# Kernel tuning notes

Measured on AMD Instinct MI355X. Metric: run time of the kernel, lower is better.

The kernel has to match this reference:

```python
import jax, jax.numpy as jnp
import numpy as np

D_MODEL = 1024
NUM_HEADS = 16
DIM_Q = 1024
DIM_K = DIM_Q // NUM_HEADS  # 64, also dim_v
B, S = 2, 2048


def setup_inputs() -> dict:
    key = jax.random.key(0)
    ks = jax.random.split(key, 11)
    sd = 0.02
    return {
        "inputs_q": jax.random.normal(ks[0], (B, S, D_MODEL), dtype=jnp.float32),
        "inputs_k": jax.random.normal(ks[1], (B, S, D_MODEL), dtype=jnp.float32),
        "inputs_v": jax.random.normal(ks[2], (B, S, D_MODEL), dtype=jnp.float32),
        "Wq": jax.random.normal(ks[3], (D_MODEL, DIM_Q), dtype=jnp.float32) * sd,
        "bq": jax.random.normal(ks[4], (DIM_Q,), dtype=jnp.float32) * sd,
        "Wk": jax.random.normal(ks[5], (D_MODEL, DIM_K), dtype=jnp.float32) * sd,
        "bk": jax.random.normal(ks[6], (DIM_K,), dtype=jnp.float32) * sd,
        "Wv": jax.random.normal(ks[7], (D_MODEL, DIM_K), dtype=jnp.float32) * sd,
        "bv": jax.random.normal(ks[8], (DIM_K,), dtype=jnp.float32) * sd,
        "Wo": jax.random.normal(ks[9], (DIM_K * NUM_HEADS, D_MODEL), dtype=jnp.float32) * sd,
        "bo": jax.random.normal(ks[10], (D_MODEL,), dtype=jnp.float32) * sd,
    }


def reference(inputs_q, inputs_k, inputs_v, Wq, bq, Wk, bk, Wv, bv, Wo, bo):
    q = inputs_q @ Wq + bq                       # [B, S, dim_q]
    k = inputs_k @ Wk + bk                       # [B, S, dim_k] (single shared head)
    v = inputs_v @ Wv + bv                       # [B, S, dim_v]
    b, n, _ = q.shape
    q = q.reshape(b, n, NUM_HEADS, DIM_K).transpose(0, 2, 1, 3)  # [B, H, N, dk]
    logits = jnp.einsum("bhnk,bmk->bhnm", q, k) / jnp.sqrt(jnp.float32(DIM_K))
    # causal mask (lower triangular keep)
    causal = jnp.tril(jnp.ones((n, k.shape[1]), dtype=bool))
    logits = jnp.where(causal[None, None], logits, -jnp.inf)
    attn = jax.nn.softmax(logits, axis=-1)
    out = jnp.einsum("bhnm,bmv->bhnv", attn, v)  # [B, H, N, dv]
    out = out.transpose(0, 2, 1, 3).reshape(b, n, NUM_HEADS * DIM_K)
    return out @ Wo + bo
```

## Files before the change

kernel.cpp:

```cpp
#include <hip/hip_runtime.h>
#include <cstdint>
#include <cstddef>

typedef unsigned short u16;
typedef __bf16 bf16x8 __attribute__((ext_vector_type(8)));
typedef float  f32x4  __attribute__((ext_vector_type(4)));
typedef float  f32x16 __attribute__((ext_vector_type(16)));
typedef unsigned u32x4 __attribute__((ext_vector_type(4)));

#define DEV __device__ __forceinline__

#define B_  2
#define S_  2048
#define DM  1024
#define H_  16
#define DK  64
#define M_  (B_ * S_)

#if __has_builtin(__builtin_amdgcn_exp2f)
#define EXP2(x) __builtin_amdgcn_exp2f(x)
#else
#define EXP2(x) exp2f(x)
#endif

constexpr size_t OFF_QBF  = 0;
constexpr size_t OFF_KF   = OFF_QBF  + (size_t)M_ * DM * 2;
constexpr size_t OFF_VF   = OFF_KF   + (size_t)M_ * DK * 2;
constexpr size_t OFF_AOBF = OFF_VF   + (size_t)M_ * DK * 2;
constexpr size_t OFF_WQT  = OFF_AOBF + (size_t)M_ * DM * 2;
constexpr size_t OFF_WOT  = OFF_WQT  + (size_t)DM * DM * 2;
constexpr size_t OFF_WKT  = OFF_WOT  + (size_t)DM * DM * 2;
constexpr size_t OFF_WVT  = OFF_WKT  + (size_t)DK * DM * 2;
constexpr size_t OFF_XQBF = OFF_WVT  + (size_t)DK * DM * 2;

DEV u16 f2bf(float f) {
  unsigned u = __float_as_uint(f);
  u += 0x7fffu + ((u >> 16) & 1u);
  return (u16)(u >> 16);
}

DEV unsigned cvtpk(float lo, float hi) {
  return (unsigned)f2bf(lo) | ((unsigned)f2bf(hi) << 16);
}

DEV unsigned cvtpk_hw(float lo, float hi) {
  unsigned r;
  asm("v_cvt_pk_bf16_f32 %0, %1, %2" : "=v"(r) : "v"(lo), "v"(hi));
  return r;
}

DEV u32x4 pack8(const float4& a, const float4& b) {
  u32x4 w;
  w[0] = cvtpk(a.x, a.y);
  w[1] = cvtpk(a.z, a.w);
  w[2] = cvtpk(b.x, b.y);
  w[3] = cvtpk(b.z, b.w);
  return w;
}

DEV void gload_lds16(const void* g, void* l) {
  __builtin_amdgcn_global_load_lds(
      (const __attribute__((address_space(1))) unsigned int*)g,
      (__attribute__((address_space(3))) unsigned int*)l, 16, 0, 0);
}

struct GemmSmem { u16 At[2][128 * 64]; u16 Bt[2][64 * 64]; };
struct KvSmem   { u16 At[64 * 32]; u16 Bt[64 * 32]; u16 stage[64][72]; };
union QkvSmem { GemmSmem g; KvSmem kv; };

__global__ __launch_bounds__(256) void prep_kernel(
    const float* __restrict__ Wq, const float* __restrict__ Wo,
    const float* __restrict__ Wk, const float* __restrict__ Wv,
    const float* __restrict__ in_q,
    u16* __restrict__ WqT, u16* __restrict__ WoT,
    u16* __restrict__ WkT, u16* __restrict__ WvT,
    u16* __restrict__ Xq) {
  const int z = blockIdx.z;
  if (z == 4) {
    const int tid = (blockIdx.y * 32 + blockIdx.x) * 256 +
                    threadIdx.y * 32 + threadIdx.x;
    const int n8 = M_ * DM / 8;
    for (int i = tid; i < n8; i += 1024 * 256) {
      float4 a = ((const float4*)in_q)[2 * i];
      float4 b = ((const float4*)in_q)[2 * i + 1];
      ((u32x4*)Xq)[i] = pack8(a, b);
    }
    return;
  }
  const float* W; u16* WT; int C;
  if (z == 0)      { W = Wq; WT = WqT; C = DM; }
  else if (z == 1) { W = Wo; WT = WoT; C = DM; }
  else if (z == 2) { W = Wk; WT = WkT; C = DK; }
  else             { W = Wv; WT = WvT; C = DK; }
  const int c0 = blockIdx.x * 32, r0 = blockIdx.y * 32;
  if (c0 >= C) return;
  __shared__ u16 tile[32][33];
  for (int i = threadIdx.y; i < 32; i += 8)
    tile[i][threadIdx.x] = f2bf(W[(size_t)(r0 + i) * C + c0 + threadIdx.x]);
  __syncthreads();
  for (int i = threadIdx.y; i < 32; i += 8)
    WT[(size_t)(c0 + i) * DM + r0 + threadIdx.x] = tile[threadIdx.x][i];
}

DEV void kvproj_dev(KvSmem& sm,
                    const float* __restrict__ X, const u16* __restrict__ WT,
                    const float* __restrict__ bias,
                    u16* __restrict__ KF, u16* __restrict__ VF,
                    int bm, int sel) {
  const int tid = threadIdx.x, wave = tid >> 6, lane = tid & 63;
  const int g = lane >> 4, c = lane & 15;
  const int wm = wave >> 1, wn = wave & 1;
  f32x4 acc[2][2] = {};

  const int row = tid >> 2, sd = tid & 3;
  const float* Asrc = X + (size_t)(bm * 64 + row) * DM + sd * 8;
  const u16* Bsrc = WT + (size_t)row * DM + ((sd ^ (row & 3)) * 8);
  u16* Adst = sm.At + row * 32 + ((sd ^ (row & 3)) * 8);

  for (int k0 = 0; k0 < DM; k0 += 32) {
    __syncthreads();
    const float4 x0 = *(const float4*)(Asrc + k0);
    const float4 x1 = *(const float4*)(Asrc + k0 + 4);
    gload_lds16(Bsrc + k0, sm.Bt + wave * 512);
    *(u32x4*)Adst = pack8(x0, x1);
    asm volatile("s_waitcnt vmcnt(0)" ::: "memory");
    __syncthreads();

    bf16x8 af[2], bfr[2];
#pragma unroll
    for (int mf = 0; mf < 2; ++mf) {
      const int ra = wm * 32 + mf * 16 + c;
      af[mf] = *(const bf16x8*)(sm.At + ra * 32 + ((g ^ (ra & 3)) * 8));
    }
#pragma unroll
    for (int nf = 0; nf < 2; ++nf) {
      const int rb = wn * 32 + nf * 16 + c;
      bfr[nf] = *(const bf16x8*)(sm.Bt + rb * 32 + ((g ^ (rb & 3)) * 8));
    }
#pragma unroll
    for (int mf = 0; mf < 2; ++mf)
#pragma unroll
      for (int nf = 0; nf < 2; ++nf)
        acc[mf][nf] = __builtin_amdgcn_mfma_f32_16x16x32_bf16(
            af[mf], bfr[nf], acc[mf][nf], 0, 0, 0);
  }

  __syncthreads();
#pragma unroll
  for (int nf = 0; nf < 2; ++nf) {
    const int col = wn * 32 + nf * 16 + c;
    const float bs = bias[col];
#pragma unroll
    for (int mf = 0; mf < 2; ++mf)
#pragma unroll
      for (int r = 0; r < 4; ++r)
        sm.stage[wm * 32 + mf * 16 + g * 4 + r][col] = f2bf(acc[mf][nf][r] + bs);
  }
  __syncthreads();

  u16* outF = (sel ? VF : KF) + (size_t)bm * 4096;
#pragma unroll
  for (int p = 0; p < 2; ++p) {
    const int id = tid + p * 256;
    const int sub = id >> 8, ks = (id >> 6) & 3, ln = id & 63;
    const int hi2 = ln >> 5, q = ln & 31;
    if (!sel) {
      const int sq = (q & ~12) | ((q & 4) << 1) | ((q & 8) >> 1);
      *(bf16x8*)&outF[id * 8] =
          *(const bf16x8*)&sm.stage[sub * 32 + sq][ks * 16 + hi2 * 8];
    } else {
      u16 tmp[8];
#pragma unroll
      for (int i = 0; i < 8; ++i)
        tmp[i] = sm.stage[ks * 16 + hi2 * 8 + i][sub * 32 + q];
      *(bf16x8*)&outF[id * 8] = *(const bf16x8*)tmp;
    }
  }
}

template <int OUT_F32>
DEV void gemm_dev(GemmSmem& sm,
                  const u16* __restrict__ A, const u16* __restrict__ BT,
                  const float* __restrict__ bias, void* __restrict__ Cout,
                  int M, int N, int K, float oscale, int bm, int bn) {
  const int tid = threadIdx.x, wave = tid >> 6, lane = tid & 63;
  const int wm = wave >> 1, wn = wave & 1;
  const int g = lane >> 4, c = lane & 15;
  f32x4 acc[4][2] = {};

  int arow[4], acol[4], brow[2], bcol[2];
#pragma unroll
  for (int i = 0; i < 4; ++i) {
    const int sid = (i * 4 + wave) * 64 + lane;
    arow[i] = sid >> 3;
    acol[i] = ((sid & 7) ^ ((sid >> 3) & 7)) * 8;
  }
#pragma unroll
  for (int i = 0; i < 2; ++i) {
    const int sid = (i * 4 + wave) * 64 + lane;
    brow[i] = sid >> 3;
    bcol[i] = ((sid & 7) ^ ((sid >> 3) & 7)) * 8;
  }
  const int nt = K >> 6;

  auto stage_g = [&](int buf, int t) {
    const int k0_ = t << 6;
#pragma unroll
    for (int i = 0; i < 4; ++i)
      gload_lds16(A + (size_t)(bm * 128 + arow[i]) * K + k0_ + acol[i],
                  &sm.At[buf][(i * 4 + wave) * 512]);
#pragma unroll
    for (int i = 0; i < 2; ++i)
      gload_lds16(BT + (size_t)(bn * 64 + brow[i]) * K + k0_ + bcol[i],
                  &sm.Bt[buf][(i * 4 + wave) * 512]);
  };

  stage_g(0, 0);
  asm volatile("s_waitcnt vmcnt(0)" ::: "memory");
  __syncthreads();

  int cur = 0;
  for (int t = 0; t < nt; ++t) {
    if (t + 1 < nt) stage_g(cur ^ 1, t + 1);
#pragma unroll
    for (int kk = 0; kk < 2; ++kk) {
      bf16x8 af[4], bfr[2];
#pragma unroll
      for (int mf = 0; mf < 4; ++mf) {
        const int row = wm * 64 + mf * 16 + c;
        af[mf] = *(const bf16x8*)(&sm.At[cur][row * 64 + ((kk * 4 + g) ^ (row & 7)) * 8]);
      }
#pragma unroll
      for (int nf = 0; nf < 2; ++nf) {
        const int row = wn * 32 + nf * 16 + c;
        bfr[nf] = *(const bf16x8*)(&sm.Bt[cur][row * 64 + ((kk * 4 + g) ^ (row & 7)) * 8]);
      }
#pragma unroll
      for (int mf = 0; mf < 4; ++mf)
#pragma unroll
        for (int nf = 0; nf < 2; ++nf)
          acc[mf][nf] = __builtin_amdgcn_mfma_f32_16x16x32_bf16(
              af[mf], bfr[nf], acc[mf][nf], 0, 0, 0);
    }
    asm volatile("s_waitcnt vmcnt(0)" ::: "memory");
    __syncthreads();
    cur ^= 1;
  }

  const int colb = bn * 64 + wn * 32 + c;
  const int rowb = bm * 128 + wm * 64 + g * 4;
#pragma unroll
  for (int nf = 0; nf < 2; ++nf) {
    float bs = bias[colb + nf * 16];
#pragma unroll
    for (int mf = 0; mf < 4; ++mf) {
#pragma unroll
      for (int r = 0; r < 4; ++r) {
        size_t idx = (size_t)(rowb + mf * 16 + r) * N + colb + nf * 16;
        float v = (acc[mf][nf][r] + bs) * oscale;
        if (OUT_F32) ((float*)Cout)[idx] = v;
        else         ((u16*)Cout)[idx]   = f2bf(v);
      }
    }
  }
}

__global__ __launch_bounds__(256) void qkv_fused_kernel(
    const u16* __restrict__ Xq, const u16* __restrict__ WqT,
    const float* __restrict__ bq, u16* __restrict__ Qbf, float qscale,
    const float* __restrict__ Xk, const float* __restrict__ Xv,
    const u16* __restrict__ WkT, const u16* __restrict__ WvT,
    const float* __restrict__ bk, const float* __restrict__ bv,
    u16* __restrict__ KF, u16* __restrict__ VF) {
  __shared__ QkvSmem sm;
  if (blockIdx.y < 16) {
    gemm_dev<0>(sm.g, Xq, WqT, bq, Qbf, M_, DM, DM, qscale,
                blockIdx.x, blockIdx.y);
  } else {
    const int id = (blockIdx.y - 16) * 32 + blockIdx.x;
    const int sel = id >> 6, bm = id & 63;
    kvproj_dev(sm.kv, sel ? Xv : Xk, sel ? WvT : WkT, sel ? bv : bk,
               KF, VF, bm, sel);
  }
}

template <int OUT_F32>
__global__ __launch_bounds__(256) void gemm_bf16_kernel(
    const u16* __restrict__ A, const u16* __restrict__ BT,
    const float* __restrict__ bias, void* __restrict__ Cout,
    int M, int N, int K, float oscale) {
  __shared__ GemmSmem sm;
  gemm_dev<OUT_F32>(sm, A, BT, bias, Cout, M, N, K, oscale,
                    blockIdx.x, blockIdx.y);
}

DEV void attn_load(const u16* kp, const u16* vp, bf16x8* kf, bf16x8* vf) {
#pragma unroll
  for (int i = 0; i < 4; ++i) {
    kf[i]     = *(const bf16x8*)(kp + i * 512);
    kf[4 + i] = *(const bf16x8*)(kp + 2048 + i * 512);
    vf[i]     = *(const bf16x8*)(vp + i * 512);
    vf[4 + i] = *(const bf16x8*)(vp + 2048 + i * 512);
  }
}

DEV void attn_comp(int t, int qrow, int hi, bool evenU, int nt,
                   const bf16x8* kf, const bf16x8* vf, const bf16x8* qf,
                   f32x16& acc0, f32x16& acc1, float& l_) {
  const int kv0 = t * 64;
  const bool diag = (t == nt - 1);
  const bool skipHi = diag && evenU;

  f32x16 sf0 = {}, sf1 = {};
  __builtin_amdgcn_s_setprio(1);
#pragma unroll
  for (int ks = 0; ks < 4; ++ks)
    sf0 = __builtin_amdgcn_mfma_f32_32x32x16_bf16(kf[ks], qf[ks], sf0, 0, 0, 0);
  if (!skipHi) {
#pragma unroll
    for (int ks = 0; ks < 4; ++ks)
      sf1 = __builtin_amdgcn_mfma_f32_32x32x16_bf16(kf[4 + ks], qf[ks], sf1, 0, 0, 0);
  }
  __builtin_amdgcn_s_setprio(0);

  if (diag) {
#pragma unroll
    for (int r = 0; r < 16; ++r) {
      const int kvl = (r & 7) + 8 * hi + 16 * (r >> 3);
      if (kv0 + kvl > qrow)      sf0[r] = -1e30f;
      if (kv0 + 32 + kvl > qrow) sf1[r] = -1e30f;
    }
  }

  float rs0 = 0.f, rs1 = 0.f;
#pragma unroll
  for (int r = 0; r < 8; ++r)  { float e = EXP2(sf0[r]); sf0[r] = e; rs0 += e; }
#pragma unroll
  for (int r = 8; r < 16; ++r) { float e = EXP2(sf0[r]); sf0[r] = e; rs1 += e; }
  if (!skipHi) {
#pragma unroll
    for (int r = 0; r < 8; ++r)  { float e = EXP2(sf1[r]); sf1[r] = e; rs0 += e; }
#pragma unroll
    for (int r = 8; r < 16; ++r) { float e = EXP2(sf1[r]); sf1[r] = e; rs1 += e; }
  }
  l_ += rs0 + rs1;

  __builtin_amdgcn_s_setprio(1);
#pragma unroll
  for (int at = 0; at < 2; ++at) {
    if (at == 1 && skipHi) break;
    const f32x16& sfv = at ? sf1 : sf0;
#pragma unroll
    for (int half = 0; half < 2; ++half) {
      const int rb = half * 8;
      u32x4 pw;
      pw[0] = cvtpk_hw(sfv[rb + 0], sfv[rb + 1]);
      pw[1] = cvtpk_hw(sfv[rb + 2], sfv[rb + 3]);
      pw[2] = cvtpk_hw(sfv[rb + 4], sfv[rb + 5]);
      pw[3] = cvtpk_hw(sfv[rb + 6], sfv[rb + 7]);
      const bf16x8 pa = __builtin_bit_cast(bf16x8, pw);
      const int ksg = at * 2 + half;
      acc0 = __builtin_amdgcn_mfma_f32_32x32x16_bf16(pa, vf[ksg], acc0, 0, 0, 0);
      acc1 = __builtin_amdgcn_mfma_f32_32x32x16_bf16(pa, vf[4 + ksg], acc1, 0, 0, 0);
    }
  }
  __builtin_amdgcn_s_setprio(0);
}

__global__ __launch_bounds__(128, 2) void attn_kernel(
    const u16* __restrict__ Q,
    const u16* __restrict__ KF,
    const u16* __restrict__ VF,
    u16* __restrict__ O) {
  __shared__ float Ll[2][32];
  __shared__ float Lacc[2][32][64];

  const int j = blockIdx.x, h = blockIdx.y, b = blockIdx.z;
  const int wave = threadIdx.x >> 6, lane = threadIdx.x & 63;
  const int q31 = lane & 31, hi = lane >> 5;

  const int u = 63 - j;
  const int qrow = u * 32 + q31;
  const int nt = (u + 2) >> 1;
  const bool evenU = !(u & 1);

  const u16* Qp = Q + (size_t)(b * S_ + qrow) * DM + h * DK;
  bf16x8 qf[4];
#pragma unroll
  for (int ks = 0; ks < 4; ++ks)
    qf[ks] = *(const bf16x8*)(Qp + ks * 16 + hi * 8);

  f32x16 acc0 = {}, acc1 = {};
  float l_ = 0.f;

  const u16* kfb = KF + (size_t)(b * 32) * 4096 + lane * 8;
  const u16* vfb = VF + (size_t)(b * 32) * 4096 + lane * 8;

  bf16x8 kA[8], vA[8], kB[8], vB[8];
  int t = wave;
  if (t < nt)
    attn_load(kfb + (size_t)t * 4096, vfb + (size_t)t * 4096, kA, vA);
  for (; t < nt; t += 4) {
    const int t1 = t + 2;
    if (t1 < nt)
      attn_load(kfb + (size_t)t1 * 4096, vfb + (size_t)t1 * 4096, kB, vB);
    attn_comp(t, qrow, hi, evenU, nt, kA, vA, qf, acc0, acc1, l_);
    if (t1 < nt) {
      const int t2 = t1 + 2;
      if (t2 < nt)
        attn_load(kfb + (size_t)t2 * 4096, vfb + (size_t)t2 * 4096, kA, vA);
      attn_comp(t1, qrow, hi, evenU, nt, kB, vB, qf, acc0, acc1, l_);
    }
  }

  l_ += __shfl_xor(l_, 32);

  if (hi == 0) Ll[wave][q31] = l_;
  __syncthreads();

#pragma unroll
  for (int r = 0; r < 16; ++r) {
    const int rr = (r & 3) + 8 * (r >> 2) + 4 * hi;
    Lacc[wave][rr][q31]      = acc0[r];
    Lacc[wave][rr][32 + q31] = acc1[r];
  }
  __syncthreads();

  const int tid = threadIdx.x;
  const int row = tid >> 2;
  const int dv0 = (tid & 3) * 16;
  const float Lr = Ll[0][row] + Ll[1][row];
  const float linv = 1.f / Lr;
  u16 ov[16];
#pragma unroll
  for (int i = 0; i < 16; ++i) {
    const float v = (Lacc[0][row][dv0 + i] + Lacc[1][row][dv0 + i]) * linv;
    ov[i] = f2bf(v);
  }
  u16* Op = O + (size_t)(b * S_ + u * 32 + row) * DM + h * DK + dv0;
  *(bf16x8*)Op       = *(const bf16x8*)ov;
  *(bf16x8*)(Op + 8) = *(const bf16x8*)(ov + 8);
}

extern "C" void kernel_launch(void* const* d_in, const int* in_sizes, int n_in,
                              void* d_out, int out_size, void* d_ws, size_t ws_size,
                              hipStream_t stream) {
  const float* in_q = (const float*)d_in[0];
  const float* in_k = (const float*)d_in[1];
  const float* in_v = (const float*)d_in[2];
  const float* Wq   = (const float*)d_in[3];
  const float* bq   = (const float*)d_in[4];
  const float* Wk   = (const float*)d_in[5];
  const float* bk   = (const float*)d_in[6];
  const float* Wv   = (const float*)d_in[7];
  const float* bv   = (const float*)d_in[8];
  const float* Wo   = (const float*)d_in[9];
  const float* bo   = (const float*)d_in[10];

  char* ws  = (char*)d_ws;
  u16* Qbf  = (u16*)(ws + OFF_QBF);
  u16* KFp  = (u16*)(ws + OFF_KF);
  u16* VFp  = (u16*)(ws + OFF_VF);
  u16* AObf = (u16*)(ws + OFF_AOBF);
  u16* WqT  = (u16*)(ws + OFF_WQT);
  u16* WoT  = (u16*)(ws + OFF_WOT);
  u16* WkT  = (u16*)(ws + OFF_WKT);
  u16* WvT  = (u16*)(ws + OFF_WVT);
  u16* Xqbf = (u16*)(ws + OFF_XQBF);

  prep_kernel<<<dim3(32, 32, 5), dim3(32, 8), 0, stream>>>(
      Wq, Wo, Wk, Wv, in_q, WqT, WoT, WkT, WvT, Xqbf);

  qkv_fused_kernel<<<dim3(32, 20), 256, 0, stream>>>(
      Xqbf, WqT, bq, Qbf, 0.125f * 1.44269504088896f,
      in_k, in_v, WkT, WvT, bk, bv, KFp, VFp);

  attn_kernel<<<dim3(64, H_, B_), 128, 0, stream>>>(Qbf, KFp, VFp, AObf);

  gemm_bf16_kernel<1><<<dim3(M_ / 128, DM / 64), 256, 0, stream>>>(
      AObf, WoT, bo, d_out, M_, DM, DM, 1.0f);
}
```

Measured before the change: 95.09 us.

## Double-buffer K/V projection GEMM with 64-wide K tiles and prefetch

Result: no change. 93.81 us (-1.4%).

```diff
diff --git a/kernel.cpp b/kernel.cpp
--- a/kernel.cpp
+++ b/kernel.cpp
@@ -65,7 +65,7 @@
 }
 
 struct GemmSmem { u16 At[2][128 * 64]; u16 Bt[2][64 * 64]; };
-struct KvSmem   { u16 At[64 * 32]; u16 Bt[64 * 32]; u16 stage[64][72]; };
+struct KvSmem   { u16 At[2][64 * 64]; u16 Bt[2][64 * 64]; u16 stage[64][72]; };
 union QkvSmem { GemmSmem g; KvSmem kv; };
 
 __global__ __launch_bounds__(256) void prep_kernel(
@@ -113,39 +113,74 @@
   f32x4 acc[2][2] = {};
 
   const int row = tid >> 2, sd = tid & 3;
-  const float* Asrc = X + (size_t)(bm * 64 + row) * DM + sd * 8;
-  const u16* Bsrc = WT + (size_t)row * DM + ((sd ^ (row & 3)) * 8);
-  u16* Adst = sm.At + row * 32 + ((sd ^ (row & 3)) * 8);
-
-  for (int k0 = 0; k0 < DM; k0 += 32) {
+  const int s0 = sd, s1 = sd + 4;
+  const float* Asrc = X + (size_t)(bm * 64 + row) * DM;
+  const int d0 = row * 64 + ((s0 ^ (row & 7)) * 8);
+  const int d1 = row * 64 + ((s1 ^ (row & 7)) * 8);
+  float4 ar0, ar1, ar2, ar3;
+
+  int brow[2], bcol[2];
+#pragma unroll
+  for (int i = 0; i < 2; ++i) {
+    const int sid = (i * 4 + wave) * 64 + lane;
+    brow[i] = sid >> 3;
+    bcol[i] = ((sid & 7) ^ ((sid >> 3) & 7)) * 8;
+  }
+
+  auto loadA = [&](int t) {
+    const float* p = Asrc + (t << 6);
+    ar0 = *(const float4*)(p + s0 * 8);
+    ar1 = *(const float4*)(p + s0 * 8 + 4);
+    ar2 = *(const float4*)(p + s1 * 8);
+    ar3 = *(const float4*)(p + s1 * 8 + 4);
+  };
+  auto writeA = [&](int buf) {
+    *(u32x4*)&sm.At[buf][d0] = pack8(ar0, ar1);
+    *(u32x4*)&sm.At[buf][d1] = pack8(ar2, ar3);
+  };
+  auto stageB = [&](int buf, int t) {
+#pragma unroll
+    for (int i = 0; i < 2; ++i)
+      gload_lds16(WT + (size_t)brow[i] * DM + (t << 6) + bcol[i],
+                  &sm.Bt[buf][(i * 4 + wave) * 512]);
+  };
+
+  const int nt = DM >> 6;
+  loadA(0);
+  stageB(0, 0);
+  asm volatile("s_waitcnt vmcnt(0)" ::: "memory");
+  writeA(0);
+  __syncthreads();
+
+  int cur = 0;
+  for (int t = 0; t < nt; ++t) {
+    if (t + 1 < nt) { stageB(cur ^ 1, t + 1); loadA(t + 1); }
+#pragma unroll
+    for (int kk = 0; kk < 2; ++kk) {
+      bf16x8 af[2], bfr[2];
+#pragma unroll
+      for (int mf = 0; mf < 2; ++mf) {
+        const int ra = wm * 32 + mf * 16 + c;
+        af[mf] = *(const bf16x8*)(&sm.At[cur][ra * 64 + ((kk * 4 + g) ^ (ra & 7)) * 8]);
+      }
+#pragma unroll
+      for (int nf = 0; nf < 2; ++nf) {
+        const int rb = wn * 32 + nf * 16 + c;
+        bfr[nf] = *(const bf16x8*)(&sm.Bt[cur][rb * 64 + ((kk * 4 + g) ^ (rb & 7)) * 8]);
+      }
+#pragma unroll
+      for (int mf = 0; mf < 2; ++mf)
+#pragma unroll
+        for (int nf = 0; nf < 2; ++nf)
+          acc[mf][nf] = __builtin_amdgcn_mfma_f32_16x16x32_bf16(
+              af[mf], bfr[nf], acc[mf][nf], 0, 0, 0);
+    }
+    asm volatile("s_waitcnt vmcnt(0)" ::: "memory");
+    if (t + 1 < nt) writeA(cur ^ 1);
     __syncthreads();
-    const float4 x0 = *(const float4*)(Asrc + k0);
-    const float4 x1 = *(const float4*)(Asrc + k0 + 4);
-    gload_lds16(Bsrc + k0, sm.Bt + wave * 512);
-    *(u32x4*)Adst = pack8(x0, x1);
-    asm volatile("s_waitcnt vmcnt(0)" ::: "memory");
-    __syncthreads();
-
-    bf16x8 af[2], bfr[2];
-#pragma unroll
-    for (int mf = 0; mf < 2; ++mf) {
-      const int ra = wm * 32 + mf * 16 + c;
-      af[mf] = *(const bf16x8*)(sm.At + ra * 32 + ((g ^ (ra & 3)) * 8));
-    }
-#pragma unroll
-    for (int nf = 0; nf < 2; ++nf) {
-      const int rb = wn * 32 + nf * 16 + c;
-      bfr[nf] = *(const bf16x8*)(sm.Bt + rb * 32 + ((g ^ (rb & 3)) * 8));
-    }
-#pragma unroll
-    for (int mf = 0; mf < 2; ++mf)
-#pragma unroll
-      for (int nf = 0; nf < 2; ++nf)
-        acc[mf][nf] = __builtin_amdgcn_mfma_f32_16x16x32_bf16(
-            af[mf], bfr[nf], acc[mf][nf], 0, 0, 0);
-  }
-
-  __syncthreads();
+    cur ^= 1;
+  }
+
 #pragma unroll
   for (int nf = 0; nf < 2; ++nf) {
     const int col = wn * 32 + nf * 16 + c;
```
